# Performance work log

Hardware: AMD Instinct MI355X
Metric: run time of the kernel (lower is better)

## Reference

```python
import jax, jax.numpy as jnp
import numpy as np

NSAMPLE = 16
GROUPS = 8  # 128 // 16 per nn.GroupNorm(C//16, C)
EPS = 1e-5


def _conv1d(w, b, x):
    # 1x1 Conv1d: w [O,C], x [B,C,N]
    return jnp.einsum('oc,bcn->bon', w, x) + b[None, :, None]


def _conv2d(w, b, x):
    # 1x1 Conv2d: w [O,C], x [B,C,N,K]
    return jnp.einsum('oc,bcnk->bonk', w, x) + b[None, :, None, None]


def _gn(x, g, b):
    # GroupNorm over (C//G, N, K) per (batch, group), as torch GroupNorm on NCHW
    B, C, N, K = x.shape
    xg = x.reshape(B, GROUPS, C // GROUPS, N, K)
    mu = xg.mean(axis=(2, 3, 4), keepdims=True)
    var = ((xg - mu) ** 2).mean(axis=(2, 3, 4), keepdims=True)
    xn = ((xg - mu) * jax.lax.rsqrt(var + EPS)).reshape(B, C, N, K)
    return xn * g[None, :, None, None] + b[None, :, None, None]


def _lrelu(x):
    return jnp.where(x >= 0, x, 0.1 * x)


def _knn_idx(xyz1, xyz2, k):
    # squared pairwise distances (monotone in torch.norm -> same top-k indices)
    s1 = jnp.sum(xyz1 * xyz1, axis=1)  # [B,N1]
    s2 = jnp.sum(xyz2 * xyz2, axis=1)  # [B,N2]
    d2 = s1[:, :, None] + s2[:, None, :] - 2.0 * jnp.einsum('bcn,bcm->bnm', xyz1, xyz2)
    return jax.lax.top_k(-d2, k)[1]  # [B,N1,K] nearest neighbors


def _group(points, idx):
    # points [B,C,N2], idx [B,N1,K] -> [B,C,N1,K]  (pointnet2 grouping_operation)
    return jax.vmap(lambda p, i: p[:, i])(points, idx)


def _cross(xyz1, xyz2, p1, p2, pos_w, pos_b, gn_g, gn_b, mlp_params):
    idx = _knn_idx(xyz1, xyz2, NSAMPLE)
    neighbor_xyz = _group(xyz2, idx)                      # [B,3,N1,K]
    direction = neighbor_xyz - xyz1[:, :, :, None]
    gp2 = _group(p2, idx)                                 # [B,C,N1,K]
    pos_feat = _conv2d(pos_w, pos_b, direction)
    new_points = _lrelu(_gn(gp2 + p1[:, :, :, None] + pos_feat, gn_g, gn_b))
    for (w, b, g, bb) in mlp_params:
        new_points = _lrelu(_gn(_conv2d(w, b, new_points), g, bb))
    return jnp.max(new_points, axis=3)                    # max-pool over K


def setup_inputs() -> dict:
    key = jax.random.key(0)
    ks = jax.random.split(key, 40)
    B, N, CIN, C = 2, 4096, 64, 128
    f32 = jnp.float32

    def w(k, o, i):
        return jax.random.normal(k, (o, i), f32) * 0.05

    inp = {
        'pc1': jax.random.normal(ks[0], (B, 3, N), f32),
        'pc2': jax.random.normal(ks[1], (B, 3, N), f32),
        'feat1': jax.random.normal(ks[2], (B, CIN, N), f32),
        'feat2': jax.random.normal(ks[3], (B, CIN, N), f32),
        't11_w': w(ks[4], C, CIN), 't11_b': jnp.zeros((C,), f32),
        't22_w': w(ks[5], C, CIN), 't22_b': jnp.zeros((C,), f32),
        'pos1_w': w(ks[6], C, 3), 'pos1_b': jnp.zeros((C,), f32),
        'gn1_g': jnp.ones((C,), f32), 'gn1_b': jnp.zeros((C,), f32),
        'm1a_w': w(ks[7], C, C), 'm1a_b': jnp.zeros((C,), f32),
        'm1a_g': jnp.ones((C,), f32), 'm1a_beta': jnp.zeros((C,), f32),
        'm1b_w': w(ks[8], C, C), 'm1b_b': jnp.zeros((C,), f32),
        'm1b_g': jnp.ones((C,), f32), 'm1b_beta': jnp.zeros((C,), f32),
        't1_w': w(ks[9], C, C), 't1_b': jnp.zeros((C,), f32),
        't2_w': w(ks[10], C, C), 't2_b': jnp.zeros((C,), f32),
        'pos2_w': w(ks[11], C, 3), 'pos2_b': jnp.zeros((C,), f32),
        'gn2_g': jnp.ones((C,), f32), 'gn2_b': jnp.zeros((C,), f32),
        'm2a_w': w(ks[12], C, C), 'm2a_b': jnp.zeros((C,), f32),
        'm2a_g': jnp.ones((C,), f32), 'm2a_beta': jnp.zeros((C,), f32),
    }
    return inp


def reference(pc1, pc2, feat1, feat2,
              t11_w, t11_b, t22_w, t22_b,
              pos1_w, pos1_b, gn1_g, gn1_b,
              m1a_w, m1a_b, m1a_g, m1a_beta,
              m1b_w, m1b_b, m1b_g, m1b_beta,
              t1_w, t1_b, t2_w, t2_b,
              pos2_w, pos2_b, gn2_g, gn2_b,
              m2a_w, m2a_b, m2a_g, m2a_beta):
    mlp1 = [(m1a_w, m1a_b, m1a_g, m1a_beta), (m1b_w, m1b_b, m1b_g, m1b_beta)]
    mlp2 = [(m2a_w, m2a_b, m2a_g, m2a_beta)]
    f1 = _conv1d(t11_w, t11_b, feat1)
    f2 = _conv1d(t22_w, t22_b, feat2)
    g1 = _conv1d(t11_w, t11_b, feat2)
    g2 = _conv1d(t22_w, t22_b, feat1)
    feat1_new = _conv1d(t1_w, t1_b, _cross(pc1, pc2, f1, f2, pos1_w, pos1_b, gn1_g, gn1_b, mlp1))
    feat2_new = _conv1d(t2_w, t2_b, _cross(pc2, pc1, g1, g2, pos1_w, pos1_b, gn1_g, gn1_b, mlp1))
    feat1_final = _cross(pc1, pc2, feat1_new, feat2_new, pos2_w, pos2_b, gn2_g, gn2_b, mlp2)
    return (feat1_new, feat2_new, feat1_final)
```

## Files before the change

### kernel.cpp

```cpp
#include <hip/hip_runtime.h>
#include <hip/hip_bf16.h>

#define NPTS 4096
#define CC   128
#define KNN  16
#define CNT_PER_GROUP 1048576.0f
#define STAT_STRIDE 1024

typedef __attribute__((ext_vector_type(8))) short bf16x8;
typedef __attribute__((ext_vector_type(8))) unsigned short u16x8;
typedef __attribute__((ext_vector_type(4))) float f32x4;
typedef unsigned short ushort_t;

static __device__ __forceinline__ ushort_t f2bf(float f) {
    __hip_bfloat16 h = __float2bfloat16(f);
    ushort_t u; __builtin_memcpy(&u, &h, 2);
    return u;
}
static __device__ __forceinline__ float bf2f(ushort_t u) {
    unsigned v = (unsigned)u << 16;
    float f; __builtin_memcpy(&f, &v, 4);
    return f;
}

__global__ void prep_kernel(const float* __restrict__ t11_w, const float* __restrict__ t22_w,
                            const float* __restrict__ t1_w,  const float* __restrict__ t2_w,
                            const float* __restrict__ m1a_w, const float* __restrict__ m1b_w,
                            const float* __restrict__ m2a_w,
                            float* __restrict__ wTt11, float* __restrict__ wTt22,
                            float* __restrict__ wTt1,  float* __restrict__ wTt2,
                            ushort_t* __restrict__ W2m1a, ushort_t* __restrict__ W2m1b,
                            ushort_t* __restrict__ W2m2a, float* __restrict__ stats) {
    int y = blockIdx.y;
    int idx = blockIdx.x * 256 + threadIdx.x;
    if (y == 7) {
        if (idx < 8 * STAT_STRIDE) stats[idx] = 0.0f;
        return;
    }
    if (y < 4) {
        const float* in; float* outp; int Cdim;
        switch (y) {
            case 0: in = t11_w; outp = wTt11; Cdim = 64; break;
            case 1: in = t22_w; outp = wTt22; Cdim = 64; break;
            case 2: in = t1_w;  outp = wTt1;  Cdim = CC; break;
            default: in = t2_w; outp = wTt2;  Cdim = CC; break;
        }
        if (idx < CC * Cdim) {
            int o = idx / Cdim, c = idx % Cdim;
            outp[c * CC + o] = in[idx];
        }
        return;
    }
    const float* in = y == 4 ? m1a_w : y == 5 ? m1b_w : m2a_w;
    ushort_t* outp  = y == 4 ? W2m1a : y == 5 ? W2m1b : W2m2a;
    if (idx < 16384) {
        int j = idx & 7, lane = (idx >> 3) & 63, coT = (idx >> 9) & 7, kb = idx >> 12;
        int k  = kb * 32 + (lane >> 4) * 8 + j;
        int co = coT * 16 + (lane & 15);
        outp[idx] = f2bf(in[co * CC + k]);
    }
}

__global__ __launch_bounds__(256) void conv64_kernel(
        const float* __restrict__ feat1, const float* __restrict__ feat2,
        const float* __restrict__ wTt11, const float* __restrict__ wTt22,
        const float* __restrict__ b11, const float* __restrict__ b22,
        float* __restrict__ f1, float* __restrict__ f2,
        float* __restrict__ g1, float* __restrict__ g2) {
    __shared__ float xs[64][68];
    int y = blockIdx.y;
    const float* x  = (y == 0 || y == 3) ? feat1 : feat2;
    const float* wT = (y == 0 || y == 2) ? wTt11 : wTt22;
    const float* bias = (y == 0 || y == 2) ? b11 : b22;
    float* outp = y == 0 ? f1 : y == 1 ? f2 : y == 2 ? g1 : g2;
    int tid = threadIdx.x;
    int n0 = blockIdx.x * 64;
    int b = n0 >> 12, nloc = n0 & 4095;
    const float* xb = x + (size_t)b * 64 * NPTS + nloc;
    #pragma unroll
    for (int i = 0; i < 16; ++i) {
        int e = tid + 256 * i;
        int ci = e >> 6, nn = e & 63;
        xs[ci][nn] = xb[(size_t)ci * NPTS + nn];
    }
    __syncthreads();
    int co = (tid & 31) * 4;
    int r0 = (tid >> 5) * 8;
    float acc[4][8];
    float4 bv = *(const float4*)&bias[co];
    #pragma unroll
    for (int j = 0; j < 8; ++j) { acc[0][j] = bv.x; acc[1][j] = bv.y; acc[2][j] = bv.z; acc[3][j] = bv.w; }
    for (int ci = 0; ci < 64; ++ci) {
        float4 wv = *(const float4*)&wT[(size_t)ci * CC + co];
        #pragma unroll
        for (int j = 0; j < 8; ++j) {
            float xv = xs[ci][r0 + j];
            acc[0][j] += wv.x * xv;
            acc[1][j] += wv.y * xv;
            acc[2][j] += wv.z * xv;
            acc[3][j] += wv.w * xv;
        }
    }
    #pragma unroll
    for (int j = 0; j < 8; ++j) {
        *(float4*)&outp[(size_t)(n0 + r0 + j) * CC + co] =
            make_float4(acc[0][j], acc[1][j], acc[2][j], acc[3][j]);
    }
}

static __device__ __forceinline__ unsigned long long sxor64(unsigned long long v, int m) {
    unsigned lo = (unsigned)__shfl_xor((int)(unsigned)v, m);
    unsigned hi = (unsigned)__shfl_xor((int)(v >> 32), m);
    return ((unsigned long long)hi << 32) | lo;
}

__global__ __launch_bounds__(512) void knn_kernel(
        const float* __restrict__ pc1, const float* __restrict__ pc2,
        int* __restrict__ idx12, int* __restrict__ idx21) {
#pragma clang fp contract(off)
    __shared__ float4 pk[NPTS];
    __shared__ unsigned long long lst[8][4][64];
    int dir = blockIdx.y;
    const float* qs = dir ? pc2 : pc1;
    const float* cs = dir ? pc1 : pc2;
    int* outIdx = dir ? idx21 : idx12;
    int tid = threadIdx.x, lane = tid & 63, wv = tid >> 6;
    int qbase = blockIdx.x * 32;
    int b = qbase >> 12;
    const float* cb = cs + (size_t)b * 3 * NPTS;
    for (int i = tid; i < NPTS; i += 512) {
        float x = cb[i], y = cb[NPTS + i], z = cb[2 * NPTS + i];
        pk[i] = make_float4(x, y, z, x * x + y * y + z * z);
    }
    __syncthreads();
    const float* qb = qs + (size_t)b * 3 * NPTS;
    int q0 = qbase + wv * 4;
    float qx[4], qy[4], qz[4], s1[4], dmin[4], T[4];
    #pragma unroll
    for (int t = 0; t < 4; ++t) {
        int n = (q0 + t) & 4095;
        qx[t] = qb[n]; qy[t] = qb[NPTS + n]; qz[t] = qb[2 * NPTS + n];
        s1[t] = qx[t] * qx[t] + qy[t] * qy[t] + qz[t] * qz[t];
        dmin[t] = 1e30f;
    }
    for (int j = 0; j < 64; ++j) {
        float4 P = pk[j * 64 + lane];
        #pragma unroll
        for (int t = 0; t < 4; ++t) {
            float dt = __builtin_fmaf(P.z, qz[t], __builtin_fmaf(P.y, qy[t], P.x * qx[t]));
            float d2 = (s1[t] + P.w) - 2.0f * dt;
            dmin[t] = fminf(dmin[t], d2);
        }
    }
    #pragma unroll
    for (int t = 0; t < 4; ++t) {
        float sv = dmin[t];
        for (int k = 2; k <= 64; k <<= 1)
            for (int j = k >> 1; j > 0; j >>= 1) {
                float o = __shfl_xor(sv, j);
                bool tmin = (((lane & k) == 0) == ((lane & j) == 0));
                sv = tmin ? fminf(sv, o) : fmaxf(sv, o);
            }
        T[t] = __shfl(sv, 15);
    }
    int base[4] = {0, 0, 0, 0};
    for (int j = 0; j < 64; ++j) {
        float4 P = pk[j * 64 + lane];
        int m = j * 64 + lane;
        #pragma unroll
        for (int t = 0; t < 4; ++t) {
            float dt = __builtin_fmaf(P.z, qz[t], __builtin_fmaf(P.y, qy[t], P.x * qx[t]));
            float d2 = (s1[t] + P.w) - 2.0f * dt;
            bool p = (d2 <= T[t]);
            unsigned long long mk = __ballot(p);
            if (p) {
                int pos = base[t] + (int)__popcll(mk & ((1ULL << lane) - 1ULL));
                unsigned u = __float_as_uint(d2);
                u ^= (unsigned)(((int)u >> 31) | 0x80000000);
                unsigned long long key = ((unsigned long long)u << 32) | (unsigned)m;
                if (pos < 64) lst[wv][t][pos] = key;
            }
            base[t] += (int)__popcll(mk);
        }
    }
    #pragma unroll
    for (int t = 0; t < 4; ++t) {
        int nT = base[t] < 64 ? base[t] : 64;
        unsigned long long key = (lane < nT) ? lst[wv][t][lane] : ~0ULL;
        for (int k = 2; k <= 64; k <<= 1)
            for (int j = k >> 1; j > 0; j >>= 1) {
                unsigned long long o = sxor64(key, j);
                bool tmin = (((lane & k) == 0) == ((lane & j) == 0));
                unsigned long long mn = key < o ? key : o;
                unsigned long long mx = key < o ? o : key;
                key = tmin ? mn : mx;
            }
        if (lane < KNN) outIdx[(size_t)(q0 + t) * KNN + lane] = (int)(unsigned)(key & 0xFFFFFFFFULL);
    }
}

__global__ void h0_kernel(const float* __restrict__ p1f, const float* __restrict__ p2f,
                          const float* __restrict__ pcA, const float* __restrict__ pcB,
                          const int* __restrict__ idx,
                          const float* __restrict__ pos_w, const float* __restrict__ pos_b,
                          ushort_t* __restrict__ buf, float* __restrict__ stats_out) {
    __shared__ float redS[128], redQ[128];
    int p = blockIdx.x;
    int b = p >> 12, n = p & 4095;
    int c = threadIdx.x;
    float pw0 = pos_w[c * 3], pw1 = pos_w[c * 3 + 1], pw2 = pos_w[c * 3 + 2];
    float pb = pos_b[c];
    float p1v = p1f[(size_t)p * CC + c];
    const float* pa = pcA + (size_t)b * 3 * NPTS;
    const float* pc = pcB + (size_t)b * 3 * NPTS;
    float qx = pa[n], qy = pa[NPTS + n], qz = pa[2 * NPTS + n];
    float S = 0.f, Q = 0.f;
    for (int k = 0; k < KNN; ++k) {
        int m = idx[(size_t)p * KNN + k];
        float dx = pc[m] - qx;
        float dy = pc[NPTS + m] - qy;
        float dz = pc[2 * NPTS + m] - qz;
        float pos = pw0 * dx + pw1 * dy + pw2 * dz + pb;
        float v = p2f[((size_t)b * NPTS + m) * CC + c] + p1v + pos;
        buf[((size_t)p * KNN + k) * CC + c] = f2bf(v);
        S += v; Q += v * v;
    }
    redS[c] = S; redQ[c] = Q;
    __syncthreads();
    if (c < 8) {
        float SS = 0.f, QQ = 0.f;
        for (int i = 0; i < 16; ++i) { SS += redS[c * 16 + i]; QQ += redQ[c * 16 + i]; }
        int s = blockIdx.x & 31;
        atomicAdd(&stats_out[s * 32 + (b * 8 + c) * 2],     SS);
        atomicAdd(&stats_out[s * 32 + (b * 8 + c) * 2 + 1], QQ);
    }
}

__global__ __launch_bounds__(256) void convgn_kernel(
        const ushort_t* __restrict__ xbuf, const float* __restrict__ stats_in,
        const float* __restrict__ gam, const float* __restrict__ bet,
        const ushort_t* __restrict__ W2, const float* __restrict__ bias,
        ushort_t* __restrict__ ybuf, float* __restrict__ stats_out) {
    __shared__ ushort_t xt[64 * 136];
    __shared__ float sc[CC], sh[CC];
    __shared__ float redS[4][8], redQ[4][8];
    int tid = threadIdx.x;
    int s0 = blockIdx.x * 64;
    int b = s0 >> 16;
    if (tid < CC) {
        int g = tid >> 4;
        float S = 0.f, Q = 0.f;
        for (int s = 0; s < 32; ++s) {
            S += stats_in[s * 32 + (b * 8 + g) * 2];
            Q += stats_in[s * 32 + (b * 8 + g) * 2 + 1];
        }
        float mu = S / CNT_PER_GROUP;
        float var = Q / CNT_PER_GROUP - mu * mu;
        float rs = rsqrtf(var + 1e-5f);
        float scale = gam[tid] * rs;
        sc[tid] = scale;
        sh[tid] = bet[tid] - mu * scale;
    }
    __syncthreads();
    #pragma unroll
    for (int j = 0; j < 4; ++j) {
        int idx = tid + 256 * j;
        int row = idx >> 4, c8 = (idx & 15) * 8;
        u16x8 vin = *(const u16x8*)&xbuf[(size_t)(s0 + row) * CC + c8];
        u16x8 vo;
        #pragma unroll
        for (int e = 0; e < 8; ++e) {
            float v = bf2f(vin[e]) * sc[c8 + e] + sh[c8 + e];
            v = v >= 0.f ? v : 0.1f * v;
            vo[e] = f2bf(v);
        }
        *(u16x8*)&xt[row * 136 + c8] = vo;
    }
    __syncthreads();
    int lane = tid & 63, wv = tid >> 6;
    int r0 = wv * 16;
    int quad = lane >> 4;
    f32x4 acc[8];
    #pragma unroll
    for (int t = 0; t < 8; ++t) acc[t] = (f32x4){0.f, 0.f, 0.f, 0.f};
    int aoff = (r0 + (lane & 15)) * 136 + quad * 8;
    #pragma unroll
    for (int kb = 0; kb < 4; ++kb) {
        bf16x8 a = *(const bf16x8*)&xt[aoff + kb * 32];
        const ushort_t* wb = W2 + (size_t)kb * 4096 + lane * 8;
        #pragma unroll
        for (int t = 0; t < 8; ++t) {
            bf16x8 bf = *(const bf16x8*)&wb[t * 512];
            acc[t] = __builtin_amdgcn_mfma_f32_16x16x32_bf16(a, bf, acc[t], 0, 0, 0);
        }
    }
    #pragma unroll
    for (int t = 0; t < 8; ++t) {
        int co = t * 16 + (lane & 15);
        float bv = bias[co];
        float S = 0.f, Q = 0.f;
        #pragma unroll
        for (int reg = 0; reg < 4; ++reg) {
            int row = s0 + r0 + quad * 4 + reg;
            float y = acc[t][reg] + bv;
            ybuf[(size_t)row * CC + co] = f2bf(y);
            S += y; Q += y * y;
        }
        #pragma unroll
        for (int off = 1; off < 64; off <<= 1) {
            S += __shfl_xor(S, off);
            Q += __shfl_xor(Q, off);
        }
        if (lane == 0) { redS[wv][t] = S; redQ[wv][t] = Q; }
    }
    __syncthreads();
    if (tid < 8) {
        float S = redS[0][tid] + redS[1][tid] + redS[2][tid] + redS[3][tid];
        float Q = redQ[0][tid] + redQ[1][tid] + redQ[2][tid] + redQ[3][tid];
        int s = blockIdx.x & 31;
        atomicAdd(&stats_out[s * 32 + (b * 8 + tid) * 2],     S);
        atomicAdd(&stats_out[s * 32 + (b * 8 + tid) * 2 + 1], Q);
    }
}

__global__ void maxpool_kernel(const ushort_t* __restrict__ ybuf, const float* __restrict__ stats,
                               const float* __restrict__ gam, const float* __restrict__ bet,
                               float* __restrict__ outb) {
    int p = blockIdx.x;
    int b = p >> 12, n = p & 4095;
    int c = threadIdx.x;
    int g = c >> 4;
    float S = 0.f, Q = 0.f;
    for (int s = 0; s < 32; ++s) {
        S += stats[s * 32 + (b * 8 + g) * 2];
        Q += stats[s * 32 + (b * 8 + g) * 2 + 1];
    }
    float mu = S / CNT_PER_GROUP;
    float var = Q / CNT_PER_GROUP - mu * mu;
    float rs = rsqrtf(var + 1e-5f);
    float scale = gam[c] * rs;
    float shift = bet[c] - mu * scale;
    float mx = -INFINITY;
    for (int k = 0; k < KNN; ++k) {
        float v = bf2f(ybuf[((size_t)p * KNN + k) * CC + c]) * scale + shift;
        v = v >= 0.f ? v : 0.1f * v;
        mx = fmaxf(mx, v);
    }
    outb[((size_t)b * CC + c) * NPTS + n] = mx;
}

__global__ void maxconv_kernel(const ushort_t* __restrict__ ybuf, const float* __restrict__ stats,
                               const float* __restrict__ gam, const float* __restrict__ bet,
                               const float* __restrict__ wT, const float* __restrict__ bias,
                               float* __restrict__ outf, float* __restrict__ outb) {
    __shared__ float mxs[CC];
    int p = blockIdx.x;
    int b = p >> 12, n = p & 4095;
    int c = threadIdx.x;
    int g = c >> 4;
    float S = 0.f, Q = 0.f;
    for (int s = 0; s < 32; ++s) {
        S += stats[s * 32 + (b * 8 + g) * 2];
        Q += stats[s * 32 + (b * 8 + g) * 2 + 1];
    }
    float mu = S / CNT_PER_GROUP;
    float var = Q / CNT_PER_GROUP - mu * mu;
    float rs = rsqrtf(var + 1e-5f);
    float scale = gam[c] * rs;
    float shift = bet[c] - mu * scale;
    float mx = -INFINITY;
    for (int k = 0; k < KNN; ++k) {
        float v = bf2f(ybuf[((size_t)p * KNN + k) * CC + c]) * scale + shift;
        v = v >= 0.f ? v : 0.1f * v;
        mx = fmaxf(mx, v);
    }
    mxs[c] = mx;
    __syncthreads();
    float acc = bias[c];
    #pragma unroll 8
    for (int ci = 0; ci < CC; ++ci)
        acc += wT[(size_t)ci * CC + c] * mxs[ci];
    outf[(size_t)p * CC + c] = acc;
    outb[((size_t)b * CC + c) * NPTS + n] = acc;
}

extern "C" void kernel_launch(void* const* d_in, const int* in_sizes, int n_in,
                              void* d_out, int out_size, void* d_ws, size_t ws_size,
                              hipStream_t stream) {
    (void)in_sizes; (void)n_in; (void)out_size; (void)ws_size;
    const float* pc1    = (const float*)d_in[0];
    const float* pc2    = (const float*)d_in[1];
    const float* feat1  = (const float*)d_in[2];
    const float* feat2  = (const float*)d_in[3];
    const float* t11_w  = (const float*)d_in[4];
    const float* t11_b  = (const float*)d_in[5];
    const float* t22_w  = (const float*)d_in[6];
    const float* t22_b  = (const float*)d_in[7];
    const float* pos1_w = (const float*)d_in[8];
    const float* pos1_b = (const float*)d_in[9];
    const float* gn1_g  = (const float*)d_in[10];
    const float* gn1_b  = (const float*)d_in[11];
    const float* m1a_w  = (const float*)d_in[12];
    const float* m1a_b  = (const float*)d_in[13];
    const float* m1a_g  = (const float*)d_in[14];
    const float* m1a_be = (const float*)d_in[15];
    const float* m1b_w  = (const float*)d_in[16];
    const float* m1b_b  = (const float*)d_in[17];
    const float* m1b_g  = (const float*)d_in[18];
    const float* m1b_be = (const float*)d_in[19];
    const float* t1_w   = (const float*)d_in[20];
    const float* t1_b   = (const float*)d_in[21];
    const float* t2_w   = (const float*)d_in[22];
    const float* t2_b   = (const float*)d_in[23];
    const float* pos2_w = (const float*)d_in[24];
    const float* pos2_b = (const float*)d_in[25];
    const float* gn2_g  = (const float*)d_in[26];
    const float* gn2_b  = (const float*)d_in[27];
    const float* m2a_w  = (const float*)d_in[28];
    const float* m2a_b  = (const float*)d_in[29];
    const float* m2a_g  = (const float*)d_in[30];
    const float* m2a_be = (const float*)d_in[31];

    float* out = (float*)d_out;
    const size_t PN = 2 * NPTS;
    const size_t PT = PN * CC;
    float* ws   = (float*)d_ws;
    float* f1   = ws;
    float* f2   = f1 + PT;
    float* g1   = f2 + PT;
    float* g2   = g1 + PT;
    float* f1n  = g2 + PT;
    float* f2n  = f1n + PT;
    int*   idx12 = (int*)(f2n + PT);
    int*   idx21 = idx12 + PN * KNN;
    float* stats = (float*)(idx21 + PN * KNN);
    float* wTt11 = stats + 8 * STAT_STRIDE;
    float* wTt22 = wTt11 + 64 * CC;
    float* wTt1  = wTt22 + 64 * CC;
    float* wTt2  = wTt1 + CC * CC;
    ushort_t* W2m1a = (ushort_t*)(wTt2 + CC * CC);
    ushort_t* W2m1b = W2m1a + 16384;
    ushort_t* W2m2a = W2m1b + 16384;
    ushort_t* bufX  = W2m2a + 16384;
    ushort_t* bufY  = bufX + (size_t)PN * KNN * CC;

    prep_kernel<<<dim3(64, 8), 256, 0, stream>>>(
        t11_w, t22_w, t1_w, t2_w, m1a_w, m1b_w, m2a_w,
        wTt11, wTt22, wTt1, wTt2, W2m1a, W2m1b, W2m2a, stats);

    conv64_kernel<<<dim3(PN / 64, 4), 256, 0, stream>>>(
        feat1, feat2, wTt11, wTt22, t11_b, t22_b, f1, f2, g1, g2);
    knn_kernel<<<dim3(PN / 32, 2), 512, 0, stream>>>(pc1, pc2, idx12, idx21);

    float* st0 = stats;
    h0_kernel<<<PN, 128, 0, stream>>>(f1, f2, pc1, pc2, idx12, pos1_w, pos1_b, bufX, st0 + 0 * STAT_STRIDE);
    convgn_kernel<<<2048, 256, 0, stream>>>(bufX, st0 + 0 * STAT_STRIDE, gn1_g, gn1_b, W2m1a, m1a_b, bufY, st0 + 1 * STAT_STRIDE);
    convgn_kernel<<<2048, 256, 0, stream>>>(bufY, st0 + 1 * STAT_STRIDE, m1a_g, m1a_be, W2m1b, m1b_b, bufX, st0 + 2 * STAT_STRIDE);
    maxconv_kernel<<<PN, 128, 0, stream>>>(bufX, st0 + 2 * STAT_STRIDE, m1b_g, m1b_be, wTt1, t1_b, f1n, out);

    h0_kernel<<<PN, 128, 0, stream>>>(g1, g2, pc2, pc1, idx21, pos1_w, pos1_b, bufX, st0 + 3 * STAT_STRIDE);
    convgn_kernel<<<2048, 256, 0, stream>>>(bufX, st0 + 3 * STAT_STRIDE, gn1_g, gn1_b, W2m1a, m1a_b, bufY, st0 + 4 * STAT_STRIDE);
    convgn_kernel<<<2048, 256, 0, stream>>>(bufY, st0 + 4 * STAT_STRIDE, m1a_g, m1a_be, W2m1b, m1b_b, bufX, st0 + 5 * STAT_STRIDE);
    maxconv_kernel<<<PN, 128, 0, stream>>>(bufX, st0 + 5 * STAT_STRIDE, m1b_g, m1b_be, wTt2, t2_b, f2n, out + PT);

    h0_kernel<<<PN, 128, 0, stream>>>(f1n, f2n, pc1, pc2, idx12, pos2_w, pos2_b, bufX, st0 + 6 * STAT_STRIDE);
    convgn_kernel<<<2048, 256, 0, stream>>>(bufX, st0 + 6 * STAT_STRIDE, gn2_g, gn2_b, W2m2a, m2a_b, bufY, st0 + 7 * STAT_STRIDE);
    maxpool_kernel<<<PN, 128, 0, stream>>>(bufY, st0 + 7 * STAT_STRIDE, m2a_g, m2a_be, out + 2 * PT);
}
```

Before: 457.2 us.

## Process 16 points per block in maxpool and maxconv kernels

The max-pool and max-pool+conv kernels now handle 16 points per 256-thread block instead of one point per 128-thread block. This amortizes the per-block GroupNorm stats reduction over 16 points and reuses each weight load across 8 points in the 128x128 conv. It also lets each thread write 8 contiguous output elements in the channel-major layout. The cost is fewer blocks (512 rather than 8192), more registers, and strided per-thread stores.

```diff
diff --git a/kernel.cpp b/kernel.cpp
--- a/kernel.cpp
+++ b/kernel.cpp
@@ -323,12 +323,14 @@
     }
 }
 
-__global__ void maxpool_kernel(const ushort_t* __restrict__ ybuf, const float* __restrict__ stats,
-                               const float* __restrict__ gam, const float* __restrict__ bet,
-                               float* __restrict__ outb) {
-    int p = blockIdx.x;
-    int b = p >> 12, n = p & 4095;
-    int c = threadIdx.x;
+__global__ __launch_bounds__(256) void maxpool_kernel(
+        const ushort_t* __restrict__ ybuf, const float* __restrict__ stats,
+        const float* __restrict__ gam, const float* __restrict__ bet,
+        float* __restrict__ outb) {
+    int p0 = blockIdx.x * 16;
+    int b = p0 >> 12, n0 = p0 & 4095;
+    int tid = threadIdx.x;
+    int c = tid & 127, half = tid >> 7;
     int g = c >> 4;
     float S = 0.f, Q = 0.f;
     for (int s = 0; s < 32; ++s) {
@@ -340,23 +342,30 @@
     float rs = rsqrtf(var + 1e-5f);
     float scale = gam[c] * rs;
     float shift = bet[c] - mu * scale;
-    float mx = -INFINITY;
-    for (int k = 0; k < KNN; ++k) {
-        float v = bf2f(ybuf[((size_t)p * KNN + k) * CC + c]) * scale + shift;
-        v = v >= 0.f ? v : 0.1f * v;
-        mx = fmaxf(mx, v);
-    }
-    outb[((size_t)b * CC + c) * NPTS + n] = mx;
-}
-
-__global__ void maxconv_kernel(const ushort_t* __restrict__ ybuf, const float* __restrict__ stats,
-                               const float* __restrict__ gam, const float* __restrict__ bet,
-                               const float* __restrict__ wT, const float* __restrict__ bias,
-                               float* __restrict__ outf, float* __restrict__ outb) {
-    __shared__ float mxs[CC];
-    int p = blockIdx.x;
-    int b = p >> 12, n = p & 4095;
-    int c = threadIdx.x;
+    float* orow = outb + ((size_t)b * CC + c) * NPTS + n0 + half * 8;
+    #pragma unroll
+    for (int j = 0; j < 8; ++j) {
+        int nl = half * 8 + j;
+        float mx = -INFINITY;
+        for (int k = 0; k < KNN; ++k) {
+            float v = bf2f(ybuf[((size_t)(p0 + nl) * KNN + k) * CC + c]) * scale + shift;
+            v = v >= 0.f ? v : 0.1f * v;
+            mx = fmaxf(mx, v);
+        }
+        orow[j] = mx;
+    }
+}
+
+__global__ __launch_bounds__(256) void maxconv_kernel(
+        const ushort_t* __restrict__ ybuf, const float* __restrict__ stats,
+        const float* __restrict__ gam, const float* __restrict__ bet,
+        const float* __restrict__ wT, const float* __restrict__ bias,
+        float* __restrict__ outf, float* __restrict__ outb) {
+    __shared__ float mxs[16][CC + 4];
+    int p0 = blockIdx.x * 16;
+    int b = p0 >> 12, n0 = p0 & 4095;
+    int tid = threadIdx.x;
+    int c = tid & 127, half = tid >> 7;
     int g = c >> 4;
     float S = 0.f, Q = 0.f;
     for (int s = 0; s < 32; ++s) {
@@ -368,20 +377,34 @@
     float rs = rsqrtf(var + 1e-5f);
     float scale = gam[c] * rs;
     float shift = bet[c] - mu * scale;
-    float mx = -INFINITY;
-    for (int k = 0; k < KNN; ++k) {
-        float v = bf2f(ybuf[((size_t)p * KNN + k) * CC + c]) * scale + shift;
-        v = v >= 0.f ? v : 0.1f * v;
-        mx = fmaxf(mx, v);
-    }
-    mxs[c] = mx;
-    __syncthreads();
-    float acc = bias[c];
-    #pragma unroll 8
-    for (int ci = 0; ci < CC; ++ci)
-        acc += wT[(size_t)ci * CC + c] * mxs[ci];
-    outf[(size_t)p * CC + c] = acc;
-    outb[((size_t)b * CC + c) * NPTS + n] = acc;
+    #pragma unroll
+    for (int j = 0; j < 8; ++j) {
+        int nl = half * 8 + j;
+        float mx = -INFINITY;
+        for (int k = 0; k < KNN; ++k) {
+            float v = bf2f(ybuf[((size_t)(p0 + nl) * KNN + k) * CC + c]) * scale + shift;
+            v = v >= 0.f ? v : 0.1f * v;
+            mx = fmaxf(mx, v);
+        }
+        mxs[nl][c] = mx;
+    }
+    __syncthreads();
+    float acc[8];
+    float bv = bias[c];
+    #pragma unroll
+    for (int j = 0; j < 8; ++j) acc[j] = bv;
+    for (int ci = 0; ci < CC; ++ci) {
+        float wv = wT[(size_t)ci * CC + c];
+        #pragma unroll
+        for (int j = 0; j < 8; ++j)
+            acc[j] += wv * mxs[half * 8 + j][ci];
+    }
+    #pragma unroll
+    for (int j = 0; j < 8; ++j)
+        outf[(size_t)(p0 + half * 8 + j) * CC + c] = acc[j];
+    float* orow = outb + ((size_t)b * CC + c) * NPTS + n0 + half * 8;
+    #pragma unroll
+    for (int j = 0; j < 8; ++j) orow[j] = acc[j];
 }
 
 extern "C" void kernel_launch(void* const* d_in, const int* in_sizes, int n_in,
@@ -456,14 +479,14 @@
     h0_kernel<<<PN, 128, 0, stream>>>(f1, f2, pc1, pc2, idx12, pos1_w, pos1_b, bufX, st0 + 0 * STAT_STRIDE);
     convgn_kernel<<<2048, 256, 0, stream>>>(bufX, st0 + 0 * STAT_STRIDE, gn1_g, gn1_b, W2m1a, m1a_b, bufY, st0 + 1 * STAT_STRIDE);
     convgn_kernel<<<2048, 256, 0, stream>>>(bufY, st0 + 1 * STAT_STRIDE, m1a_g, m1a_be, W2m1b, m1b_b, bufX, st0 + 2 * STAT_STRIDE);
-    maxconv_kernel<<<PN, 128, 0, stream>>>(bufX, st0 + 2 * STAT_STRIDE, m1b_g, m1b_be, wTt1, t1_b, f1n, out);
+    maxconv_kernel<<<PN / 16, 256, 0, stream>>>(bufX, st0 + 2 * STAT_STRIDE, m1b_g, m1b_be, wTt1, t1_b, f1n, out);
 
     h0_kernel<<<PN, 128, 0, stream>>>(g1, g2, pc2, pc1, idx21, pos1_w, pos1_b, bufX, st0 + 3 * STAT_STRIDE);
     convgn_kernel<<<2048, 256, 0, stream>>>(bufX, st0 + 3 * STAT_STRIDE, gn1_g, gn1_b, W2m1a, m1a_b, bufY, st0 + 4 * STAT_STRIDE);
     convgn_kernel<<<2048, 256, 0, stream>>>(bufY, st0 + 4 * STAT_STRIDE, m1a_g, m1a_be, W2m1b, m1b_b, bufX, st0 + 5 * STAT_STRIDE);
-    maxconv_kernel<<<PN, 128, 0, stream>>>(bufX, st0 + 5 * STAT_STRIDE, m1b_g, m1b_be, wTt2, t2_b, f2n, out + PT);
+    maxconv_kernel<<<PN / 16, 256, 0, stream>>>(bufX, st0 + 5 * STAT_STRIDE, m1b_g, m1b_be, wTt2, t2_b, f2n, out + PT);
 
     h0_kernel<<<PN, 128, 0, stream>>>(f1n, f2n, pc1, pc2, idx12, pos2_w, pos2_b, bufX, st0 + 6 * STAT_STRIDE);
     convgn_kernel<<<2048, 256, 0, stream>>>(bufX, st0 + 6 * STAT_STRIDE, gn2_g, gn2_b, W2m2a, m2a_b, bufY, st0 + 7 * STAT_STRIDE);
-    maxpool_kernel<<<PN, 128, 0, stream>>>(bufY, st0 + 7 * STAT_STRIDE, m2a_g, m2a_be, out + 2 * PT);
-}
+    maxpool_kernel<<<PN / 16, 256, 0, stream>>>(bufY, st0 + 7 * STAT_STRIDE, m2a_g, m2a_be, out + 2 * PT);
+}
```

New measurement: 397.9 us. 1.15x faster.
